# Optimization experiments

Measured on AMD Instinct MI355X. Metric: run time of the kernel, lower is better.

The kernel has to match this reference:

```python
import jax, jax.numpy as jnp
import numpy as np

B, S, D, H = 4, 2048, 2048, 16
Dh = D // H
BASE = 10000.0


def _rope_tables(seq_len, head_dim, dtype=jnp.float32):
    inv_freq = 1.0 / (BASE ** (jnp.arange(0, head_dim, 2, dtype=jnp.float32) / head_dim))
    t = jnp.arange(seq_len, dtype=jnp.float32)
    freqs = jnp.outer(t, inv_freq)              # [S, Dh/2]
    emb = jnp.concatenate([freqs, freqs], -1)   # [S, Dh]
    return jnp.cos(emb).astype(dtype), jnp.sin(emb).astype(dtype)


def _rotate_half(x):
    d = x.shape[-1] // 2
    return jnp.concatenate([-x[..., d:], x[..., :d]], axis=-1)


def setup_inputs() -> dict:
    key = jax.random.key(0)
    ks = jax.random.split(key, 5)
    std = D ** -0.5
    x = jax.random.normal(ks[0], (B, S, D), jnp.float32)
    Wq = jax.random.normal(ks[1], (D, D), jnp.float32) * std
    Wk = jax.random.normal(ks[2], (D, D), jnp.float32) * std
    Wv = jax.random.normal(ks[3], (D, D), jnp.float32) * std
    Wo = jax.random.normal(ks[4], (D, D), jnp.float32) * std
    attn_mask = jnp.triu(jnp.ones((S, S), dtype=bool), k=1)  # True = masked (causal)
    return {"x": x, "attn_mask": attn_mask, "Wq": Wq, "Wk": Wk, "Wv": Wv, "Wo": Wo}


def reference(x, attn_mask, Wq, Wk, Wv, Wo):
    b, s, d = x.shape
    # projections (nn.Linear: x @ W.T), split heads -> [B, H, S, Dh]
    q = (x @ Wq.T).reshape(b, s, H, Dh).transpose(0, 2, 1, 3)
    k = (x @ Wk.T).reshape(b, s, H, Dh).transpose(0, 2, 1, 3)
    v = (x @ Wv.T).reshape(b, s, H, Dh).transpose(0, 2, 1, 3)
    cos, sin = _rope_tables(s, Dh, x.dtype)     # [S, Dh]
    q = q * cos + _rotate_half(q) * sin
    k = k * cos + _rotate_half(k) * sin
    scale = Dh ** -0.5
    scores = jnp.einsum('bhqd,bhkd->bhqk', q, k) * scale
    scores = jnp.where(attn_mask[None, None, :, :], -jnp.inf, scores)
    weights = jax.nn.softmax(scores, axis=-1)
    out = jnp.einsum('bhqk,bhkd->bhqd', weights, v)
    out = out.transpose(0, 2, 1, 3).reshape(b, s, d)
    return out @ Wo.T
```

## Files before the change

kernel.cpp:

```cpp
#include <hip/hip_runtime.h>
#include <cstdint>
#include <cmath>

#define NB 4
#define NS 2048
#define ND 2048
#define NH 16
#define NDH 128
#define NM (NB*NS)

typedef unsigned short u16;
typedef __bf16 bf16x8 __attribute__((ext_vector_type(8)));
typedef u16    u16x8  __attribute__((ext_vector_type(8)));
typedef u16    u16x4  __attribute__((ext_vector_type(4)));
typedef float  f32x4  __attribute__((ext_vector_type(4)));
typedef float  f32x16 __attribute__((ext_vector_type(16)));
typedef unsigned u32x4_t __attribute__((ext_vector_type(4)));

__device__ __forceinline__ u16 f2bf(float f) {
  unsigned u = __float_as_uint(f);
  u += 0x7fffu + ((u >> 16) & 1u);
  return (u16)(u >> 16);
}
__device__ __forceinline__ float bf2f(u16 h) {
  return __uint_as_float(((unsigned)h) << 16);
}
__device__ __forceinline__ void gld16(const void* g, void* l) {
  __builtin_amdgcn_global_load_lds((__attribute__((address_space(1))) void*)g,
                                   (__attribute__((address_space(3))) void*)l,
                                   16, 0, 0);
}
__device__ __forceinline__ f32x4 mfma_bf16(bf16x8 a, bf16x8 b, f32x4 c) {
  return __builtin_amdgcn_mfma_f32_16x16x32_bf16(a, b, c, 0, 0, 0);
}
__device__ __forceinline__ f32x16 mfma32_bf16(bf16x8 a, bf16x8 b, f32x16 c) {
  return __builtin_amdgcn_mfma_f32_32x32x16_bf16(a, b, c, 0, 0, 0);
}
__device__ __forceinline__ unsigned cvtpk(float lo, float hi) {
  unsigned r;
  asm("v_cvt_pk_bf16_f32 %0, %1, %2" : "=v"(r) : "v"(lo), "v"(hi));
  return r;
}
__device__ __forceinline__ void p32swap(unsigned &a, unsigned &b) {
  asm volatile("v_permlane32_swap_b32 %0, %1" : "+v"(a), "+v"(b));
}

__global__ void cvt_bf16_kernel(const float* __restrict__ in, u16* __restrict__ out, int n8) {
  int i = blockIdx.x * 256 + threadIdx.x;
  if (i >= n8) return;
  const float4* p = (const float4*)in + (size_t)i * 2;
  float4 a = p[0], b = p[1];
  u16x8 r;
  r[0]=f2bf(a.x); r[1]=f2bf(a.y); r[2]=f2bf(a.z); r[3]=f2bf(a.w);
  r[4]=f2bf(b.x); r[5]=f2bf(b.y); r[6]=f2bf(b.z); r[7]=f2bf(b.w);
  ((u16x8*)out)[i] = r;
}

__global__ void rope_tables_kernel(float* __restrict__ cosT, float* __restrict__ sinT) {
  int s = blockIdx.x, d = threadIdx.x;
  double inv = pow(10000.0, -(double)d / 64.0);
  float ang = (float)((double)s * inv);
  cosT[s*64 + d] = cosf(ang);
  sinT[s*64 + d] = sinf(ang);
}

__global__ void rope_apply_kernel(u16* __restrict__ X, const float* __restrict__ cosT,
                                  const float* __restrict__ sinT) {
  int idx = blockIdx.x * 256 + threadIdx.x;
  int pc = idx & 7, h = (idx >> 3) & (NH - 1), m = idx >> 7;
  int s = m & (NS - 1);
  int d0 = pc * 8;
  size_t base = (size_t)m * ND + h * NDH + d0;
  u16x8 v0 = *(const u16x8*)(X + base);
  u16x8 v1 = *(const u16x8*)(X + base + 64);
  u16x8 r0, r1;
#pragma unroll
  for (int j = 0; j < 8; ++j) {
    float c  = cosT[s*64 + d0 + j];
    float sn = sinT[s*64 + d0 + j];
    float x0 = bf2f(v0[j]), x1 = bf2f(v1[j]);
    r0[j] = f2bf(x0 * c - x1 * sn);
    r1[j] = f2bf(x1 * c + x0 * sn);
  }
  *(u16x8*)(X + base)      = r0;
  *(u16x8*)(X + base + 64) = r1;
}

#define G_PHASE(BUF, KS, MH, LOADB, STAGE) do {                                   \
  bf16x8 af[4];                                                                   \
  _Pragma("unroll")                                                               \
  for (int mf = 0; mf < 4; ++mf)                                                  \
    af[mf] = *(const bf16x8*)(Asb + (BUF)*32768 + (KS)*16384 + arow + ((MH)*4+mf)*1024); \
  if (LOADB) {                                                                    \
    _Pragma("unroll")                                                             \
    for (int nf = 0; nf < 4; ++nf)                                                \
      bfr[nf] = *(const bf16x8*)(Bsb + (BUF)*32768 + (KS)*16384 + brow + nf*1024); \
  }                                                                               \
  STAGE;                                                                          \
  asm volatile("s_waitcnt vmcnt(8)" ::: "memory");                                \
  __builtin_amdgcn_sched_barrier(0);                                              \
  __builtin_amdgcn_s_barrier();                                                   \
  __builtin_amdgcn_s_setprio(1);                                                  \
  _Pragma("unroll")                                                               \
  for (int mf = 0; mf < 4; ++mf)                                                  \
    _Pragma("unroll")                                                             \
    for (int nf = 0; nf < 4; ++nf)                                                \
      acc[(MH)*4+mf][nf] = mfma_bf16(af[mf], bfr[nf], acc[(MH)*4+mf][nf]);        \
  __builtin_amdgcn_s_setprio(0);                                                  \
  __builtin_amdgcn_s_barrier();                                                   \
} while (0)

template <typename OutT>
__global__ __launch_bounds__(512, 1) void gemm256_kernel(
    const u16* __restrict__ A, const u16* __restrict__ Bw, OutT* __restrict__ C,
    int Nd, int Kd) {
  __shared__ __align__(16) char Asb[65536];
  __shared__ __align__(16) char Bsb[65536];
  int tid = threadIdx.x;
  int wave = tid >> 6, lane = tid & 63;
  int li = lane & 15, lg = lane >> 4;
  int wr = wave >> 2, wc = wave & 3;
  int NTn = Nd >> 8;
  int cpx = (int)gridDim.x >> 3;
  int bid = (int)blockIdx.x;
  int swz = (bid & 7) * cpx + (bid >> 3);
  int m0 = (swz / NTn) << 8, n0 = (swz % NTn) << 8;

  int rswz = (lg * 16) ^ ((li & 3) << 4);
  int arow = (wr * 128 + li) * 64 + rswz;
  int brow = (wc *  64 + li) * 64 + rswz;

  int srow = wave * 16 + (lane >> 2);
  int scswz = ((lane & 3) * 16) ^ ((srow & 3) << 4);
  size_t rowB = (size_t)Kd * 2;
  const char* Asrc = (const char*)A + (size_t)(m0 + srow) * rowB + scswz;
  const char* Bsrc = (const char*)Bw + (size_t)(n0 + srow) * rowB + scswz;
  char* Adst = Asb + wave * 1024;
  char* Bdst = Bsb + wave * 1024;
  size_t half2 = rowB << 7;

  auto stageA = [&](int buf, int ks, int tile) {
    const char* s = Asrc + (size_t)tile * 128 + ks * 64;
    char* d = Adst + buf * 32768 + ks * 16384;
    gld16(s, d);
    gld16(s + half2, d + 8192);
  };
  auto stageB = [&](int buf, int ks, int tile) {
    const char* s = Bsrc + (size_t)tile * 128 + ks * 64;
    char* d = Bdst + buf * 32768 + ks * 16384;
    gld16(s, d);
    gld16(s + half2, d + 8192);
  };

  f32x4 acc[8][4] = {};
  bf16x8 bfr[4];

  int NKT = Kd >> 6;
  int NIT = NKT >> 1;

  stageA(0, 0, 0); stageA(0, 1, 0); stageB(0, 0, 0); stageB(0, 1, 0);
  stageA(1, 0, 1); stageB(1, 0, 1);
  asm volatile("s_waitcnt vmcnt(4)" ::: "memory");
  __builtin_amdgcn_sched_barrier(0);
  __builtin_amdgcn_s_barrier();

  for (int j = 0; j < NIT; ++j) {
    int t1  = 2*j + 1;
    int tn0 = (2*j + 2) & (NKT - 1);
    int tn1 = (2*j + 3) & (NKT - 1);
    G_PHASE(0, 0, 0, true,  { stageA(1, 1, t1);  });
    G_PHASE(0, 0, 1, false, { stageB(1, 1, t1);  });
    G_PHASE(0, 1, 1, true,  { stageA(0, 0, tn0); });
    G_PHASE(0, 1, 0, false, { stageB(0, 0, tn0); });
    G_PHASE(1, 0, 0, true,  { stageA(0, 1, tn0); });
    G_PHASE(1, 0, 1, false, { stageB(0, 1, tn0); });
    G_PHASE(1, 1, 1, true,  { stageA(1, 0, tn1); });
    G_PHASE(1, 1, 0, false, { stageB(1, 0, tn1); });
  }
  asm volatile("s_waitcnt vmcnt(0)" ::: "memory");

  int rbase = m0 + wr*128 + lg*4;
  int cbase = n0 + wc*64 + li;
#pragma unroll
  for (int am = 0; am < 8; ++am)
#pragma unroll
    for (int nf = 0; nf < 4; ++nf)
#pragma unroll
      for (int r = 0; r < 4; ++r) {
        size_t off = (size_t)(rbase + am*16 + r) * Nd + (cbase + nf*16);
        if constexpr (sizeof(OutT) == 2) C[off] = f2bf(acc[am][nf][r]);
        else                             C[off] = acc[am][nf][r];
      }
}

__global__ __launch_bounds__(512, 2) void flash_attn_kernel(
    const u16* __restrict__ Q, const u16* __restrict__ K, const u16* __restrict__ V,
    u16* __restrict__ O) {
  __shared__ __align__(16) u16 Ks[2*64*128];
  __shared__ __align__(16) u16 Vt[2*128*64];
  int tid = threadIdx.x, wv = tid >> 6, lane = tid & 63;
  int ql = lane & 31, hi = lane >> 5;
  int b = blockIdx.x >> 4, h = blockIdx.x & 15;
  int qt = (int)gridDim.y - 1 - (int)blockIdx.y;
  int q0 = qt << 8;
  int qw = q0 + wv*32;
  int qa = qw + ql;
  int swzl = (ql & 7) << 4;
  const float qscale = 0.08838834764831845f * 1.4426950408889634f;

  bf16x8 qf[8];
  {
    const u16* qp = Q + (size_t)(b*NS + qa) * ND + h*NDH + hi*8;
#pragma unroll
    for (int ds = 0; ds < 8; ++ds) {
      u16x8 t = *(const u16x8*)(qp + ds*16);
      u16x8 r;
#pragma unroll
      for (int j = 0; j < 8; ++j) r[j] = f2bf(bf2f(t[j]) * qscale);
      qf[ds] = *(bf16x8*)&r;
    }
  }
  f32x16 o0 = {}, o1 = {}, o2 = {}, o3 = {};
  float m_run = -INFINITY, l_run = 0.f;

  const char* Kg = (const char*)(K + (size_t)b*NS*ND + h*NDH);
  const char* Vg = (const char*)(V + (size_t)b*NS*ND + h*NDH);
  const int ROWB = ND * 2;

  int p   = tid & 31;
  int kvg = tid >> 5;

  auto issueKV = [&](int kv0, int buf, unsigned (&dlo)[4], unsigned (&dhi)[4]) {
    const char* vrow = Vg + (size_t)(kv0 + kvg*4) * ROWB;
#pragma unroll
    for (int j = 0; j < 4; ++j) {
      dlo[j] = *(const unsigned*)(vrow + j*ROWB + p*4);
      dhi[j] = *(const unsigned*)(vrow + j*ROWB + 128 + p*4);
    }
    char* ksb = (char*)Ks + buf*16384;
#pragma unroll
    for (int c = 0; c < 2; ++c) {
      int s = c*8192 + wv*1024 + lane*16;
      int row = s >> 8;
      int within = (s & 255) ^ ((row & 7) << 4);
      gld16(Kg + (size_t)(kv0 + row)*ROWB + within, ksb + c*8192 + wv*1024);
    }
    __builtin_amdgcn_sched_barrier(0);
  };

  auto dostep = [&](int kv0, int buf, const unsigned (&dlo)[4], const unsigned (&dhi)[4],
                    bool hasNext) {
    if (hasNext) asm volatile("s_waitcnt vmcnt(10)" ::: "memory");
    else         asm volatile("s_waitcnt vmcnt(0)"  ::: "memory");
    __builtin_amdgcn_sched_barrier(0);
    __builtin_amdgcn_s_barrier();
    __builtin_amdgcn_sched_barrier(0);

    char* vtb = (char*)Vt + buf*16384;
    const char* ksb = (const char*)Ks + buf*16384;

    {
      u16x4 rA, rB, rC, rD;
#pragma unroll
      for (int j = 0; j < 4; ++j) {
        rA[j] = (u16)dlo[j]; rB[j] = (u16)(dlo[j] >> 16);
        rC[j] = (u16)dhi[j]; rD[j] = (u16)(dhi[j] >> 16);
      }
      int a0 = ((2*p   )*128 + kvg*8) ^ (((2*p  ) & 7) << 4);
      int a1 = ((2*p+ 1)*128 + kvg*8) ^ (((2*p+1) & 7) << 4);
      int a2 = ((2*p+64)*128 + kvg*8) ^ (((2*p  ) & 7) << 4);
      int a3 = ((2*p+65)*128 + kvg*8) ^ (((2*p+1) & 7) << 4);
      *(u16x4*)(vtb + a0) = rA;
      *(u16x4*)(vtb + a1) = rB;
      *(u16x4*)(vtb + a2) = rC;
      *(u16x4*)(vtb + a3) = rD;
    }

    f32x16 p0 = {}, p1 = {};
    __builtin_amdgcn_s_setprio(1);
#pragma unroll
    for (int ds = 0; ds < 8; ++ds) {
      bf16x8 kf0 = *(const bf16x8*)(ksb + ((ql*256 + ds*32 + hi*16) ^ swzl));
      p0 = mfma32_bf16(kf0, qf[ds], p0);
      bf16x8 kf1 = *(const bf16x8*)(ksb + (((32+ql)*256 + ds*32 + hi*16) ^ swzl) + 0);
      p1 = mfma32_bf16(kf1, qf[ds], p1);
    }
    __builtin_amdgcn_s_setprio(0);

    if (kv0 + 63 > qw) {
      int thresh = qa - kv0 - 4*hi;
#pragma unroll
      for (int r = 0; r < 16; ++r) {
        int c0 = (r & 3) + 8*(r >> 2);
        p0[r] = (c0      > thresh) ? -INFINITY : p0[r];
        p1[r] = (c0 + 32 > thresh) ? -INFINITY : p1[r];
      }
    }

    float mx[16];
#pragma unroll
    for (int r = 0; r < 16; ++r) mx[r] = fmaxf(p0[r], p1[r]);
#pragma unroll
    for (int s = 8; s > 0; s >>= 1)
#pragma unroll
      for (int r = 0; r < 8; ++r) if (r < s) mx[r] = fmaxf(mx[r], mx[r + s]);
    float pmax = fmaxf(mx[0], __shfl_xor(mx[0], 32, 64));

    if (!__all(pmax <= m_run + 8.f)) {
      float mn = fmaxf(m_run, pmax);
      float corr = __builtin_amdgcn_exp2f(m_run - mn);
      m_run = mn; l_run *= corr;
#pragma unroll
      for (int r = 0; r < 16; ++r) {
        float cw = __shfl(corr, (r & 3) + 8*(r >> 2) + 4*hi, 64);
        o0[r] *= cw; o1[r] *= cw; o2[r] *= cw; o3[r] *= cw;
      }
    }

    float sm[16];
#pragma unroll
    for (int r = 0; r < 16; ++r) {
      p0[r] = __builtin_amdgcn_exp2f(p0[r] - m_run);
      p1[r] = __builtin_amdgcn_exp2f(p1[r] - m_run);
      sm[r] = p0[r] + p1[r];
    }
#pragma unroll
    for (int s = 8; s > 0; s >>= 1)
#pragma unroll
      for (int r = 0; r < 8; ++r) if (r < s) sm[r] += sm[r + s];
    l_run += sm[0] + __shfl_xor(sm[0], 32, 64);

    bf16x8 pa0, pa1, pa2, pa3;
#define MKPA(P, B, OUT) {                              \
      unsigned a0 = cvtpk(P[(B)+0], P[(B)+1]);         \
      unsigned b0 = cvtpk(P[(B)+4], P[(B)+5]);         \
      p32swap(a0, b0);                                 \
      unsigned a1 = cvtpk(P[(B)+2], P[(B)+3]);         \
      unsigned b1 = cvtpk(P[(B)+6], P[(B)+7]);         \
      p32swap(a1, b1);                                 \
      u32x4_t w; w[0]=a0; w[1]=a1; w[2]=b0; w[3]=b1;   \
      OUT = *(bf16x8*)&w; }
    MKPA(p0, 0, pa0)
    MKPA(p0, 8, pa1)
    MKPA(p1, 0, pa2)
    MKPA(p1, 8, pa3)
#undef MKPA

    asm volatile("s_waitcnt lgkmcnt(0)" ::: "memory");
    __builtin_amdgcn_sched_barrier(0);
    __builtin_amdgcn_s_barrier();
    __builtin_amdgcn_sched_barrier(0);

    __builtin_amdgcn_s_setprio(1);
#define PVT(OT, T) {                                                        \
      _Pragma("unroll")                                                     \
      for (int ks = 0; ks < 4; ++ks) {                                      \
        int a = ((((T)*32 + ql)*128 + ks*32 + hi*16) ^ swzl);               \
        bf16x8 vf = *(const bf16x8*)(vtb + a);                              \
        OT = mfma32_bf16(ks==0?pa0:ks==1?pa1:ks==2?pa2:pa3, vf, OT);        \
      } }
    PVT(o0, 0)
    PVT(o1, 1)
    PVT(o2, 2)
    PVT(o3, 3)
#undef PVT
    __builtin_amdgcn_s_setprio(0);
  };

  int nt = 4*qt + 4;
  unsigned dloA[4], dhiA[4], dloB[4], dhiB[4];
  issueKV(0, 0, dloA, dhiA);
  for (int t = 0; ; t += 2) {
    bool h1 = (t+1 < nt);
    if (h1) issueKV((t+1)*64, 1, dloB, dhiB);
    dostep(t*64, 0, dloA, dhiA, h1);
    if (!h1) break;
    bool h2 = (t+2 < nt);
    if (h2) issueKV((t+2)*64, 0, dloA, dhiA);
    dostep((t+1)*64, 1, dloB, dhiB, h2);
    if (!h2) break;
  }

  float inv = 1.0f / l_run;
#pragma unroll
  for (int r = 0; r < 16; ++r) {
    int crow = (r & 3) + 8*(r >> 2) + 4*hi;
    float iv = __shfl(inv, crow, 64);
    size_t base = (size_t)(b*NS + qw + crow) * ND + h*NDH + ql;
    O[base +  0] = f2bf(o0[r] * iv);
    O[base + 32] = f2bf(o1[r] * iv);
    O[base + 64] = f2bf(o2[r] * iv);
    O[base + 96] = f2bf(o3[r] * iv);
  }
}

extern "C" void kernel_launch(void* const* d_in, const int* in_sizes, int n_in,
                              void* d_out, int out_size, void* d_ws, size_t ws_size,
                              hipStream_t stream) {
  const float* x  = (const float*)d_in[0];
  const float* Wq = (const float*)d_in[2];
  const float* Wk = (const float*)d_in[3];
  const float* Wv = (const float*)d_in[4];
  const float* Wo = (const float*)d_in[5];

  char* ws = (char*)d_ws;
  const size_t SZ_MD = (size_t)NM * ND * 2;
  const size_t SZ_W  = (size_t)ND * ND * 2;
  u16* xb  = (u16*)(ws);
  u16* Qb  = (u16*)(ws + SZ_MD);
  u16* Kb  = (u16*)(ws + 2*SZ_MD);
  u16* Vb  = (u16*)(ws + 3*SZ_MD);
  u16* Ab  = (u16*)(ws + 4*SZ_MD);
  u16* Wqb = (u16*)(ws + 5*SZ_MD);
  u16* Wkb = (u16*)(ws + 5*SZ_MD + SZ_W);
  u16* Wvb = (u16*)(ws + 5*SZ_MD + 2*SZ_W);
  u16* Wob = (u16*)(ws + 5*SZ_MD + 3*SZ_W);
  float* cosT = (float*)(ws + 5*SZ_MD + 4*SZ_W);
  float* sinT = (float*)(ws + 5*SZ_MD + 4*SZ_W + (size_t)NS*64*4);
  size_t needed = 5*SZ_MD + 4*SZ_W + 2*(size_t)NS*64*4;
  if (ws_size < needed) return;

  {
    int n8 = (NM * ND) / 8;
    cvt_bf16_kernel<<<(n8 + 255)/256, 256, 0, stream>>>(x, xb, n8);
    int w8 = (ND * ND) / 8;
    cvt_bf16_kernel<<<(w8 + 255)/256, 256, 0, stream>>>(Wq, Wqb, w8);
    cvt_bf16_kernel<<<(w8 + 255)/256, 256, 0, stream>>>(Wk, Wkb, w8);
    cvt_bf16_kernel<<<(w8 + 255)/256, 256, 0, stream>>>(Wv, Wvb, w8);
    cvt_bf16_kernel<<<(w8 + 255)/256, 256, 0, stream>>>(Wo, Wob, w8);
  }
  rope_tables_kernel<<<NS, 64, 0, stream>>>(cosT, sinT);

  const int GEMM_GRID = (NM/256) * (ND/256);
  gemm256_kernel<u16><<<GEMM_GRID, 512, 0, stream>>>(xb, Wqb, Qb, ND, ND);
  gemm256_kernel<u16><<<GEMM_GRID, 512, 0, stream>>>(xb, Wkb, Kb, ND, ND);
  gemm256_kernel<u16><<<GEMM_GRID, 512, 0, stream>>>(xb, Wvb, Vb, ND, ND);

  {
    int nthr = NM * NH * 8;
    rope_apply_kernel<<<nthr/256, 256, 0, stream>>>(Qb, cosT, sinT);
    rope_apply_kernel<<<nthr/256, 256, 0, stream>>>(Kb, cosT, sinT);
  }

  flash_attn_kernel<<<dim3(NB*NH, NS/256), 512, 0, stream>>>(Qb, Kb, Vb, Ab);

  gemm256_kernel<float><<<GEMM_GRID, 512, 0, stream>>>(Ab, Wob, (float*)d_out, ND, ND);
}
```

Baseline: 436.7 us.

## Switch GEMM to 32x32 MFMA tiles and fuse QKV projections into one launch

The GEMM kernel now uses 32x32x16 bf16 MFMA fragments instead of 16x16x32, which cuts the LDS fragment reads per MFMA FLOP. The Q, K and V projections are merged into a single 768-block launch that selects weight and output by block index. The vmcnt wait is relaxed to fire every fourth phase with one barrier per phase, and launch bounds are raised to two blocks per CU. The risks are register pressure under the higher occupancy target and LDS capacity limiting how many blocks can be co-resident.

```diff
diff --git a/kernel.cpp b/kernel.cpp
--- a/kernel.cpp
+++ b/kernel.cpp
@@ -29,9 +29,6 @@
   __builtin_amdgcn_global_load_lds((__attribute__((address_space(1))) void*)g,
                                    (__attribute__((address_space(3))) void*)l,
                                    16, 0, 0);
-}
-__device__ __forceinline__ f32x4 mfma_bf16(bf16x8 a, bf16x8 b, f32x4 c) {
-  return __builtin_amdgcn_mfma_f32_16x16x32_bf16(a, b, c, 0, 0, 0);
 }
 __device__ __forceinline__ f32x16 mfma32_bf16(bf16x8 a, bf16x8 b, f32x16 c) {
   return __builtin_amdgcn_mfma_f32_32x32x16_bf16(a, b, c, 0, 0, 0);
@@ -86,54 +83,43 @@
   *(u16x8*)(X + base + 64) = r1;
 }
 
-#define G_PHASE(BUF, KS, MH, LOADB, STAGE) do {                                   \
-  bf16x8 af[4];                                                                   \
-  _Pragma("unroll")                                                               \
-  for (int mf = 0; mf < 4; ++mf)                                                  \
-    af[mf] = *(const bf16x8*)(Asb + (BUF)*32768 + (KS)*16384 + arow + ((MH)*4+mf)*1024); \
-  if (LOADB) {                                                                    \
-    _Pragma("unroll")                                                             \
-    for (int nf = 0; nf < 4; ++nf)                                                \
-      bfr[nf] = *(const bf16x8*)(Bsb + (BUF)*32768 + (KS)*16384 + brow + nf*1024); \
-  }                                                                               \
+#define BARX do { __builtin_amdgcn_s_barrier(); __builtin_amdgcn_sched_barrier(0); } while (0)
+#define VM4  do { asm volatile("s_waitcnt vmcnt(4)" ::: "memory"); \
+                  __builtin_amdgcn_sched_barrier(0); } while (0)
+#define GP(BUF, KS, MH, LOADB, WAITV, STAGE) do {                                 \
+  bf16x8 afr[2][2];                                                               \
+  rdA(afr, BUF, KS, MH);                                                          \
+  if (LOADB) rdB(bfr, BUF, KS);                                                   \
   STAGE;                                                                          \
-  asm volatile("s_waitcnt vmcnt(8)" ::: "memory");                                \
-  __builtin_amdgcn_sched_barrier(0);                                              \
-  __builtin_amdgcn_s_barrier();                                                   \
-  __builtin_amdgcn_s_setprio(1);                                                  \
-  _Pragma("unroll")                                                               \
-  for (int mf = 0; mf < 4; ++mf)                                                  \
-    _Pragma("unroll")                                                             \
-    for (int nf = 0; nf < 4; ++nf)                                                \
-      acc[(MH)*4+mf][nf] = mfma_bf16(af[mf], bfr[nf], acc[(MH)*4+mf][nf]);        \
-  __builtin_amdgcn_s_setprio(0);                                                  \
-  __builtin_amdgcn_s_barrier();                                                   \
+  mm(afr, bfr, MH);                                                               \
+  if (WAITV) VM4;                                                                 \
+  BARX;                                                                           \
 } while (0)
 
 template <typename OutT>
-__global__ __launch_bounds__(512, 1) void gemm256_kernel(
-    const u16* __restrict__ A, const u16* __restrict__ Bw, OutT* __restrict__ C,
+__global__ __launch_bounds__(512, 2) void gemm256_kernel(
+    const u16* __restrict__ A,
+    const u16* __restrict__ B0, const u16* __restrict__ B1, const u16* __restrict__ B2,
+    OutT* __restrict__ C0, OutT* __restrict__ C1, OutT* __restrict__ C2,
     int Nd, int Kd) {
   __shared__ __align__(16) char Asb[65536];
   __shared__ __align__(16) char Bsb[65536];
   int tid = threadIdx.x;
   int wave = tid >> 6, lane = tid & 63;
-  int li = lane & 15, lg = lane >> 4;
+  int ql = lane & 31, hi = lane >> 5;
   int wr = wave >> 2, wc = wave & 3;
+  int w  = (int)blockIdx.x >> 8;
+  int tb = (int)blockIdx.x & 255;
+  const u16* Bw = (w == 0) ? B0 : (w == 1) ? B1 : B2;
+  OutT*      C  = (w == 0) ? C0 : (w == 1) ? C1 : C2;
   int NTn = Nd >> 8;
-  int cpx = (int)gridDim.x >> 3;
-  int bid = (int)blockIdx.x;
-  int swz = (bid & 7) * cpx + (bid >> 3);
+  int swz = (tb & 7) * 32 + (tb >> 3);
   int m0 = (swz / NTn) << 8, n0 = (swz % NTn) << 8;
-
-  int rswz = (lg * 16) ^ ((li & 3) << 4);
-  int arow = (wr * 128 + li) * 64 + rswz;
-  int brow = (wc *  64 + li) * 64 + rswz;
 
   int srow = wave * 16 + (lane >> 2);
   int scswz = ((lane & 3) * 16) ^ ((srow & 3) << 4);
   size_t rowB = (size_t)Kd * 2;
-  const char* Asrc = (const char*)A + (size_t)(m0 + srow) * rowB + scswz;
+  const char* Asrc = (const char*)A  + (size_t)(m0 + srow) * rowB + scswz;
   const char* Bsrc = (const char*)Bw + (size_t)(n0 + srow) * rowB + scswz;
   char* Adst = Asb + wave * 1024;
   char* Bdst = Bsb + wave * 1024;
@@ -152,8 +138,42 @@
     gld16(s + half2, d + 8192);
   };
 
-  f32x4 acc[8][4] = {};
-  bf16x8 bfr[4];
+  f32x16 acc[4][2] = {};
+  bf16x8 bfr[2][2];
+
+  auto rdA = [&](bf16x8 (&dst)[2][2], int buf, int ks, int mh) {
+#pragma unroll
+    for (int rf = 0; rf < 2; ++rf) {
+      int row = wr*128 + mh*64 + rf*32 + ql;
+      int rs = (row & 3) << 4;
+#pragma unroll
+      for (int kst = 0; kst < 2; ++kst)
+        dst[rf][kst] = *(const bf16x8*)(Asb + buf*32768 + ks*16384 + row*64
+                                        + ((kst*32 + hi*16) ^ rs));
+    }
+  };
+  auto rdB = [&](bf16x8 (&dst)[2][2], int buf, int ks) {
+#pragma unroll
+    for (int cf = 0; cf < 2; ++cf) {
+      int row = wc*64 + cf*32 + ql;
+      int rs = (row & 3) << 4;
+#pragma unroll
+      for (int kst = 0; kst < 2; ++kst)
+        dst[cf][kst] = *(const bf16x8*)(Bsb + buf*32768 + ks*16384 + row*64
+                                        + ((kst*32 + hi*16) ^ rs));
+    }
+  };
+  auto mm = [&](bf16x8 (&a)[2][2], bf16x8 (&bf_)[2][2], int mh) {
+    __builtin_amdgcn_s_setprio(1);
+#pragma unroll
+    for (int kst = 0; kst < 2; ++kst)
+#pragma unroll
+      for (int rf = 0; rf < 2; ++rf)
+#pragma unroll
+        for (int cf = 0; cf < 2; ++cf)
+          acc[mh*2+rf][cf] = mfma32_bf16(a[rf][kst], bf_[cf][kst], acc[mh*2+rf][cf]);
+    __builtin_amdgcn_s_setprio(0);
+  };
 
   int NKT = Kd >> 6;
   int NIT = NKT >> 1;
@@ -162,34 +182,35 @@
   stageA(1, 0, 1); stageB(1, 0, 1);
   asm volatile("s_waitcnt vmcnt(4)" ::: "memory");
   __builtin_amdgcn_sched_barrier(0);
-  __builtin_amdgcn_s_barrier();
+  BARX;
 
   for (int j = 0; j < NIT; ++j) {
     int t1  = 2*j + 1;
     int tn0 = (2*j + 2) & (NKT - 1);
     int tn1 = (2*j + 3) & (NKT - 1);
-    G_PHASE(0, 0, 0, true,  { stageA(1, 1, t1);  });
-    G_PHASE(0, 0, 1, false, { stageB(1, 1, t1);  });
-    G_PHASE(0, 1, 1, true,  { stageA(0, 0, tn0); });
-    G_PHASE(0, 1, 0, false, { stageB(0, 0, tn0); });
-    G_PHASE(1, 0, 0, true,  { stageA(0, 1, tn0); });
-    G_PHASE(1, 0, 1, false, { stageB(0, 1, tn0); });
-    G_PHASE(1, 1, 1, true,  { stageA(1, 0, tn1); });
-    G_PHASE(1, 1, 0, false, { stageB(1, 0, tn1); });
+    GP(0, 0, 0, true,  false, { stageA(1, 1, t1);  });
+    GP(0, 0, 1, false, false, { stageB(1, 1, t1);  });
+    GP(0, 1, 1, true,  false, { stageA(0, 0, tn0); });
+    GP(0, 1, 0, false, true,  { stageB(0, 0, tn0); });
+    GP(1, 0, 0, true,  false, { stageA(0, 1, tn0); });
+    GP(1, 0, 1, false, false, { stageB(0, 1, tn0); });
+    GP(1, 1, 1, true,  false, { stageA(1, 0, tn1); });
+    GP(1, 1, 0, false, true,  { stageB(1, 0, tn1); });
   }
   asm volatile("s_waitcnt vmcnt(0)" ::: "memory");
 
-  int rbase = m0 + wr*128 + lg*4;
-  int cbase = n0 + wc*64 + li;
-#pragma unroll
-  for (int am = 0; am < 8; ++am)
-#pragma unroll
-    for (int nf = 0; nf < 4; ++nf)
-#pragma unroll
-      for (int r = 0; r < 4; ++r) {
-        size_t off = (size_t)(rbase + am*16 + r) * Nd + (cbase + nf*16);
-        if constexpr (sizeof(OutT) == 2) C[off] = f2bf(acc[am][nf][r]);
-        else                             C[off] = acc[am][nf][r];
+  int rbase = m0 + wr*128;
+  int cbase = n0 + wc*64 + ql;
+#pragma unroll
+  for (int g = 0; g < 4; ++g)
+#pragma unroll
+    for (int cf = 0; cf < 2; ++cf)
+#pragma unroll
+      for (int r = 0; r < 16; ++r) {
+        int crow = (r & 3) + 8*(r >> 2) + 4*hi;
+        size_t off = (size_t)(rbase + g*32 + crow) * Nd + (cbase + cf*32);
+        if constexpr (sizeof(OutT) == 2) C[off] = f2bf(acc[g][cf][r]);
+        else                             C[off] = acc[g][cf][r];
       }
 }
 
@@ -282,7 +303,7 @@
     for (int ds = 0; ds < 8; ++ds) {
       bf16x8 kf0 = *(const bf16x8*)(ksb + ((ql*256 + ds*32 + hi*16) ^ swzl));
       p0 = mfma32_bf16(kf0, qf[ds], p0);
-      bf16x8 kf1 = *(const bf16x8*)(ksb + (((32+ql)*256 + ds*32 + hi*16) ^ swzl) + 0);
+      bf16x8 kf1 = *(const bf16x8*)(ksb + (((32+ql)*256 + ds*32 + hi*16) ^ swzl));
       p1 = mfma32_bf16(kf1, qf[ds], p1);
     }
     __builtin_amdgcn_s_setprio(0);
@@ -431,10 +452,8 @@
   }
   rope_tables_kernel<<<NS, 64, 0, stream>>>(cosT, sinT);
 
-  const int GEMM_GRID = (NM/256) * (ND/256);
-  gemm256_kernel<u16><<<GEMM_GRID, 512, 0, stream>>>(xb, Wqb, Qb, ND, ND);
-  gemm256_kernel<u16><<<GEMM_GRID, 512, 0, stream>>>(xb, Wkb, Kb, ND, ND);
-  gemm256_kernel<u16><<<GEMM_GRID, 512, 0, stream>>>(xb, Wvb, Vb, ND, ND);
+  gemm256_kernel<u16><<<3*256, 512, 0, stream>>>(xb, Wqb, Wkb, Wvb,
+                                                 Qb, Kb, Vb, ND, ND);
 
   {
     int nthr = NM * NH * 8;
@@ -444,5 +463,6 @@
 
   flash_attn_kernel<<<dim3(NB*NH, NS/256), 512, 0, stream>>>(Qb, Kb, Vb, Ab);
 
-  gemm256_kernel<float><<<GEMM_GRID, 512, 0, stream>>>(Ab, Wob, (float*)d_out, ND, ND);
-}
+  gemm256_kernel<float><<<256, 512, 0, stream>>>(Ab, Wob, nullptr, nullptr,
+                                                 (float*)d_out, nullptr, nullptr, ND, ND);
+}
```

New measurement: 474.2 us. 1.09x slower.

## Batch QKV projections into one launch and restructure GEMM barrier and swizzle scheme

Applied to the files above, without the earlier changes.

The three Q/K/V projection GEMMs become a single launch: the block index selects which weight and output to use, and the Wo projection reuses the same kernel. Each GEMM phase now waits on memory and barriers after its MFMAs, and only waits for outstanding loads on two of the eight phases instead of every phase. The LDS XOR swizzles in the GEMM and in the attention V-transpose buffer change to reduce bank conflicts. Launch bounds are raised to two blocks per CU, which tightens the register budget for the 128-float accumulator and risks spills, even though the LDS footprint likely still limits each CU to one block.

```diff
diff --git a/kernel.cpp b/kernel.cpp
--- a/kernel.cpp
+++ b/kernel.cpp
@@ -86,7 +86,10 @@
   *(u16x8*)(X + base + 64) = r1;
 }
 
-#define G_PHASE(BUF, KS, MH, LOADB, STAGE) do {                                   \
+#define BARX do { __builtin_amdgcn_s_barrier(); __builtin_amdgcn_sched_barrier(0); } while (0)
+#define VM4  do { asm volatile("s_waitcnt vmcnt(4)" ::: "memory"); \
+                  __builtin_amdgcn_sched_barrier(0); } while (0)
+#define GP(BUF, KS, MH, LOADB, WAITV, STAGE) do {                                 \
   bf16x8 af[4];                                                                   \
   _Pragma("unroll")                                                               \
   for (int mf = 0; mf < 4; ++mf)                                                  \
@@ -97,9 +100,6 @@
       bfr[nf] = *(const bf16x8*)(Bsb + (BUF)*32768 + (KS)*16384 + brow + nf*1024); \
   }                                                                               \
   STAGE;                                                                          \
-  asm volatile("s_waitcnt vmcnt(8)" ::: "memory");                                \
-  __builtin_amdgcn_sched_barrier(0);                                              \
-  __builtin_amdgcn_s_barrier();                                                   \
   __builtin_amdgcn_s_setprio(1);                                                  \
   _Pragma("unroll")                                                               \
   for (int mf = 0; mf < 4; ++mf)                                                  \
@@ -107,12 +107,15 @@
     for (int nf = 0; nf < 4; ++nf)                                                \
       acc[(MH)*4+mf][nf] = mfma_bf16(af[mf], bfr[nf], acc[(MH)*4+mf][nf]);        \
   __builtin_amdgcn_s_setprio(0);                                                  \
-  __builtin_amdgcn_s_barrier();                                                   \
+  if (WAITV) VM4;                                                                 \
+  BARX;                                                                           \
 } while (0)
 
 template <typename OutT>
-__global__ __launch_bounds__(512, 1) void gemm256_kernel(
-    const u16* __restrict__ A, const u16* __restrict__ Bw, OutT* __restrict__ C,
+__global__ __launch_bounds__(512, 2) void gemm256_kernel(
+    const u16* __restrict__ A,
+    const u16* __restrict__ B0, const u16* __restrict__ B1, const u16* __restrict__ B2,
+    OutT* __restrict__ C0, OutT* __restrict__ C1, OutT* __restrict__ C2,
     int Nd, int Kd) {
   __shared__ __align__(16) char Asb[65536];
   __shared__ __align__(16) char Bsb[65536];
@@ -120,20 +123,22 @@
   int wave = tid >> 6, lane = tid & 63;
   int li = lane & 15, lg = lane >> 4;
   int wr = wave >> 2, wc = wave & 3;
+  int w  = (int)blockIdx.x >> 8;
+  int tb = (int)blockIdx.x & 255;
+  const u16* Bw = (w == 0) ? B0 : (w == 1) ? B1 : B2;
+  OutT*      C  = (w == 0) ? C0 : (w == 1) ? C1 : C2;
   int NTn = Nd >> 8;
-  int cpx = (int)gridDim.x >> 3;
-  int bid = (int)blockIdx.x;
-  int swz = (bid & 7) * cpx + (bid >> 3);
+  int swz = (tb & 7) * 32 + (tb >> 3);
   int m0 = (swz / NTn) << 8, n0 = (swz % NTn) << 8;
 
-  int rswz = (lg * 16) ^ ((li & 3) << 4);
+  int rswz = (lg * 16) ^ (((li >> 1) & 3) << 4);
   int arow = (wr * 128 + li) * 64 + rswz;
   int brow = (wc *  64 + li) * 64 + rswz;
 
   int srow = wave * 16 + (lane >> 2);
-  int scswz = ((lane & 3) * 16) ^ ((srow & 3) << 4);
+  int scswz = ((lane & 3) * 16) ^ (((srow >> 1) & 3) << 4);
   size_t rowB = (size_t)Kd * 2;
-  const char* Asrc = (const char*)A + (size_t)(m0 + srow) * rowB + scswz;
+  const char* Asrc = (const char*)A  + (size_t)(m0 + srow) * rowB + scswz;
   const char* Bsrc = (const char*)Bw + (size_t)(n0 + srow) * rowB + scswz;
   char* Adst = Asb + wave * 1024;
   char* Bdst = Bsb + wave * 1024;
@@ -162,20 +167,20 @@
   stageA(1, 0, 1); stageB(1, 0, 1);
   asm volatile("s_waitcnt vmcnt(4)" ::: "memory");
   __builtin_amdgcn_sched_barrier(0);
-  __builtin_amdgcn_s_barrier();
+  BARX;
 
   for (int j = 0; j < NIT; ++j) {
     int t1  = 2*j + 1;
     int tn0 = (2*j + 2) & (NKT - 1);
     int tn1 = (2*j + 3) & (NKT - 1);
-    G_PHASE(0, 0, 0, true,  { stageA(1, 1, t1);  });
-    G_PHASE(0, 0, 1, false, { stageB(1, 1, t1);  });
-    G_PHASE(0, 1, 1, true,  { stageA(0, 0, tn0); });
-    G_PHASE(0, 1, 0, false, { stageB(0, 0, tn0); });
-    G_PHASE(1, 0, 0, true,  { stageA(0, 1, tn0); });
-    G_PHASE(1, 0, 1, false, { stageB(0, 1, tn0); });
-    G_PHASE(1, 1, 1, true,  { stageA(1, 0, tn1); });
-    G_PHASE(1, 1, 0, false, { stageB(1, 0, tn1); });
+    GP(0, 0, 0, true,  false, { stageA(1, 1, t1);  });
+    GP(0, 0, 1, false, false, { stageB(1, 1, t1);  });
+    GP(0, 1, 1, true,  false, { stageA(0, 0, tn0); });
+    GP(0, 1, 0, false, true,  { stageB(0, 0, tn0); });
+    GP(1, 0, 0, true,  false, { stageA(0, 1, tn0); });
+    GP(1, 0, 1, false, false, { stageB(0, 1, tn0); });
+    GP(1, 1, 1, true,  false, { stageA(1, 0, tn1); });
+    GP(1, 1, 0, false, true,  { stageB(1, 0, tn1); });
   }
   asm volatile("s_waitcnt vmcnt(0)" ::: "memory");
 
@@ -206,6 +211,7 @@
   int qw = q0 + wv*32;
   int qa = qw + ql;
   int swzl = (ql & 7) << 4;
+  int vswz = ((ql >> 1) & 7) << 4;
   const float qscale = 0.08838834764831845f * 1.4426950408889634f;
 
   bf16x8 qf[8];
@@ -266,10 +272,11 @@
         rA[j] = (u16)dlo[j]; rB[j] = (u16)(dlo[j] >> 16);
         rC[j] = (u16)dhi[j]; rD[j] = (u16)(dhi[j] >> 16);
       }
-      int a0 = ((2*p   )*128 + kvg*8) ^ (((2*p  ) & 7) << 4);
-      int a1 = ((2*p+ 1)*128 + kvg*8) ^ (((2*p+1) & 7) << 4);
-      int a2 = ((2*p+64)*128 + kvg*8) ^ (((2*p  ) & 7) << 4);
-      int a3 = ((2*p+65)*128 + kvg*8) ^ (((2*p+1) & 7) << 4);
+      int ws = (p & 7) << 4;
+      int a0 = ((2*p   )*128 + kvg*8) ^ ws;
+      int a1 = ((2*p+ 1)*128 + kvg*8) ^ ws;
+      int a2 = ((2*p+64)*128 + kvg*8) ^ ws;
+      int a3 = ((2*p+65)*128 + kvg*8) ^ ws;
       *(u16x4*)(vtb + a0) = rA;
       *(u16x4*)(vtb + a1) = rB;
       *(u16x4*)(vtb + a2) = rC;
@@ -282,7 +289,7 @@
     for (int ds = 0; ds < 8; ++ds) {
       bf16x8 kf0 = *(const bf16x8*)(ksb + ((ql*256 + ds*32 + hi*16) ^ swzl));
       p0 = mfma32_bf16(kf0, qf[ds], p0);
-      bf16x8 kf1 = *(const bf16x8*)(ksb + (((32+ql)*256 + ds*32 + hi*16) ^ swzl) + 0);
+      bf16x8 kf1 = *(const bf16x8*)(ksb + (((32+ql)*256 + ds*32 + hi*16) ^ swzl));
       p1 = mfma32_bf16(kf1, qf[ds], p1);
     }
     __builtin_amdgcn_s_setprio(0);
@@ -355,7 +362,7 @@
 #define PVT(OT, T) {                                                        \
       _Pragma("unroll")                                                     \
       for (int ks = 0; ks < 4; ++ks) {                                      \
-        int a = ((((T)*32 + ql)*128 + ks*32 + hi*16) ^ swzl);               \
+        int a = ((((T)*32 + ql)*128 + ks*32 + hi*16) ^ vswz);               \
         bf16x8 vf = *(const bf16x8*)(vtb + a);                              \
         OT = mfma32_bf16(ks==0?pa0:ks==1?pa1:ks==2?pa2:pa3, vf, OT);        \
       } }
@@ -431,10 +438,8 @@
   }
   rope_tables_kernel<<<NS, 64, 0, stream>>>(cosT, sinT);
 
-  const int GEMM_GRID = (NM/256) * (ND/256);
-  gemm256_kernel<u16><<<GEMM_GRID, 512, 0, stream>>>(xb, Wqb, Qb, ND, ND);
-  gemm256_kernel<u16><<<GEMM_GRID, 512, 0, stream>>>(xb, Wkb, Kb, ND, ND);
-  gemm256_kernel<u16><<<GEMM_GRID, 512, 0, stream>>>(xb, Wvb, Vb, ND, ND);
+  gemm256_kernel<u16><<<3*256, 512, 0, stream>>>(xb, Wqb, Wkb, Wvb,
+                                                 Qb, Kb, Vb, ND, ND);
 
   {
     int nthr = NM * NH * 8;
@@ -444,5 +449,6 @@
 
   flash_attn_kernel<<<dim3(NB*NH, NS/256), 512, 0, stream>>>(Qb, Kb, Vb, Ab);
 
-  gemm256_kernel<float><<<GEMM_GRID, 512, 0, stream>>>(Ab, Wob, (float*)d_out, ND, ND);
-}
+  gemm256_kernel<float><<<256, 512, 0, stream>>>(Ab, Wob, nullptr, nullptr,
+                                                 (float*)d_out, nullptr, nullptr, ND, ND);
+}
```

Measured after the change: 419.2 us. -4.0%, faster.
